# Optimization experiments

Measured on AMD Instinct MI355X. Metric: run time of the kernel, lower is better.

Reference implementation:

```python
import jax, jax.numpy as jnp
import numpy as np

N = 100_000
E = 1_600_000
D_IN = 128
D_OUT = 128
LN_EPS = 1e-5


def mean_agg(x, src, dst, deg):
    # out[dst] += x[src]; out /= deg  (scatter-mean over incoming edges)
    summed = jax.ops.segment_sum(x[src], dst, num_segments=N)
    return summed / deg[:, None]


def setup_inputs() -> dict:
    key = jax.random.key(0)
    ks = jax.random.split(key, 8)
    h = jax.random.normal(ks[0], (N, D_IN), dtype=jnp.float32)
    edge_index_mp = jax.random.randint(ks[1], (2, E), 0, N, dtype=jnp.int64)
    # deg = in-degree of each node (count of edges with dst == i), clamped to >= 1
    deg_mp = jax.ops.segment_sum(jnp.ones((E,), jnp.float32), edge_index_mp[1], num_segments=N)
    deg_mp = jnp.maximum(deg_mp, 1.0)
    scale = 1.0 / np.sqrt(D_IN)
    W_self = jax.random.uniform(ks[2], (D_OUT, D_IN), jnp.float32, -scale, scale)
    W_nb1 = jax.random.uniform(ks[3], (D_OUT, D_IN), jnp.float32, -scale, scale)
    W_hp = jax.random.uniform(ks[4], (D_OUT, D_IN), jnp.float32, -scale, scale)
    W_nb2 = jax.random.uniform(ks[5], (D_OUT, D_IN), jnp.float32, -scale, scale)
    bias = jnp.zeros((D_OUT,), jnp.float32)
    branch_logits = jnp.zeros((4,), jnp.float32)
    ln_gamma = jnp.ones((D_OUT,), jnp.float32)
    ln_beta = jnp.zeros((D_OUT,), jnp.float32)
    return {
        "h": h, "edge_index_mp": edge_index_mp, "deg_mp": deg_mp,
        "W_self": W_self, "W_nb1": W_nb1, "W_hp": W_hp, "W_nb2": W_nb2,
        "bias": bias, "branch_logits": branch_logits,
        "ln_gamma": ln_gamma, "ln_beta": ln_beta,
    }


def reference(h, edge_index_mp, deg_mp, W_self, W_nb1, W_hp, W_nb2,
              bias, branch_logits, ln_gamma, ln_beta):
    src, dst = edge_index_mp[0], edge_index_mp[1]
    nb1 = mean_agg(h, src, dst, deg_mp)          # 1-hop mean
    nb2 = mean_agg(nb1, src, dst, deg_mp)        # 2-hop mean
    hp = h - nb1                                  # high-pass branch
    scales = 2.0 * jax.nn.sigmoid(branch_logits)
    z = (scales[0] * (h @ W_self.T)
         + scales[1] * (nb1 @ W_nb1.T)
         + scales[2] * (hp @ W_hp.T)
         + scales[3] * (nb2 @ W_nb2.T)
         + bias)
    mu = jnp.mean(z, axis=-1, keepdims=True)
    var = jnp.var(z, axis=-1, keepdims=True)
    return (z - mu) * jax.lax.rsqrt(var + LN_EPS) * ln_gamma + ln_beta
```

## Files before the change

### kernel.cpp

```cpp
#include <hip/hip_runtime.h>

#define NN 100000
#define NE 1600000
#define D 128
#define KTOT 384
#define LN_EPS 1e-5f

#define PITCH_US 200
#define PITCH_DW 100
#define GM 64

#define SCAN_CHUNK 2048
#define NSB 49

#define NBK 196
#define BCAP 10240

#define FB_SCAN1   0
#define FB_WEIGHTS 49
#define FB_BIN     113
#define FB_PREP    895
#define FB_TOTAL   4020

#define WS_OFF_OFF   0
#define WS_OFF_CUR   401408
#define WS_OFF_BSUM  802816
#define WS_OFF_GCUR  803072
#define WS_OFF_WCBF  804096
#define WS_OFF_ESRC  967680
#define WS_OFF_H16   7768064
#define WS_OFF_NB1   33368064
#define WS_OFF_GBUF  33368064

typedef __attribute__((ext_vector_type(8))) _Float16 f16x8;
typedef __attribute__((ext_vector_type(2))) _Float16 f16x2;
typedef __attribute__((ext_vector_type(4))) float f32x4;
typedef __attribute__((ext_vector_type(2))) unsigned int u32x2;

__device__ __forceinline__ unsigned short f2h(float f) {
    _Float16 h = (_Float16)f;
    unsigned short s; __builtin_memcpy(&s, &h, 2); return s;
}
__device__ __forceinline__ f16x2 u2h2(unsigned u) {
    f16x2 h; __builtin_memcpy(&h, &u, 4); return h;
}
__device__ __forceinline__ unsigned pk2(float a, float b) {
    return (unsigned)f2h(a) | ((unsigned)f2h(b) << 16);
}

__global__ __launch_bounds__(256) void k_front(
    const float* __restrict__ deg, int* __restrict__ off, int* __restrict__ bsum,
    const float* __restrict__ Ws, const float* __restrict__ W1,
    const float* __restrict__ Whp, const float* __restrict__ W2,
    const float* __restrict__ logits, unsigned short* __restrict__ wcbf,
    const int* __restrict__ src, const int* __restrict__ dst,
    int* __restrict__ gcur, int2* __restrict__ gbuf,
    const float* __restrict__ h, unsigned int* __restrict__ h16) {
    __shared__ int lds[256];
    __shared__ int bcnt[NBK];
    __shared__ int bbase[NBK];
    const int b = blockIdx.x;
    const int t = threadIdx.x;

    if (b < FB_WEIGHTS) {
        int base = b * SCAN_CHUNK + t * 8;
        int v[8];
        if (base < NN) {
            float4 a0 = reinterpret_cast<const float4*>(deg + base)[0];
            float4 a1 = reinterpret_cast<const float4*>(deg + base)[1];
            v[0] = __float2int_rn(a0.x); v[1] = __float2int_rn(a0.y);
            v[2] = __float2int_rn(a0.z); v[3] = __float2int_rn(a0.w);
            v[4] = __float2int_rn(a1.x); v[5] = __float2int_rn(a1.y);
            v[6] = __float2int_rn(a1.z); v[7] = __float2int_rn(a1.w);
        } else {
            #pragma unroll
            for (int j = 0; j < 8; ++j) v[j] = 0;
        }
        int s = 0;
        #pragma unroll
        for (int j = 0; j < 8; ++j) s += v[j];
        lds[t] = s;
        __syncthreads();
        for (int ofs = 1; ofs < 256; ofs <<= 1) {
            int x = (t >= ofs) ? lds[t - ofs] : 0;
            __syncthreads();
            lds[t] += x;
            __syncthreads();
        }
        int excl = (t == 0) ? 0 : lds[t - 1];
        #pragma unroll
        for (int j = 0; j < 8; ++j) { off[base + j] = excl; excl += v[j]; }
        if (t == 255) bsum[b] = lds[255];
    } else if (b < FB_BIN) {
        int idx = (b - FB_WEIGHTS) * 256 + t;
        int o = idx >> 7, k = idx & 127;
        float s0 = 2.f / (1.f + __expf(-logits[0]));
        float s1 = 2.f / (1.f + __expf(-logits[1]));
        float s2 = 2.f / (1.f + __expf(-logits[2]));
        float s3 = 2.f / (1.f + __expf(-logits[3]));
        unsigned short b1 = f2h(s0 * Ws[idx] + s2 * Whp[idx]);
        unsigned short b2 = f2h(s1 * W1[idx] - s2 * Whp[idx]);
        unsigned short b3 = f2h(s3 * W2[idx]);
        size_t base = (size_t)o * KTOT + k;
        wcbf[base]       = b1;
        wcbf[base + 128] = b2;
        wcbf[base + 256] = b3;
    } else if (b < FB_PREP) {
        if (t < NBK) bcnt[t] = 0;
        __syncthreads();
        int e0 = (b - FB_BIN) * 2048;
        int s[8], d[8], r[8];
        #pragma unroll
        for (int it = 0; it < 8; ++it) {
            int e = e0 + it * 256 + t;
            bool ok = e < NE;
            s[it] = ok ? src[e] : 0;
            d[it] = ok ? dst[e] : -1;
            r[it] = ok ? atomicAdd(&bcnt[d[it] >> 9], 1) : 0;
        }
        __syncthreads();
        if (t < NBK) bbase[t] = atomicAdd(&gcur[t], bcnt[t]);
        __syncthreads();
        #pragma unroll
        for (int it = 0; it < 8; ++it) {
            if (d[it] >= 0) {
                int bk = d[it] >> 9;
                gbuf[(size_t)bk * BCAP + bbase[bk] + r[it]] = make_int2(s[it], d[it]);
            }
        }
    } else {
        int g2 = (b - FB_PREP) * 256 + t;
        const float4* hv = reinterpret_cast<const float4*>(h) + (size_t)g2 * 4;
        float4 a = hv[0], bb = hv[1], c = hv[2], dd = hv[3];
        uint4 o0, o1;
        o0.x = pk2(a.x, a.y);   o0.y = pk2(a.z, a.w);
        o0.z = pk2(bb.x, bb.y); o0.w = pk2(bb.z, bb.w);
        o1.x = pk2(c.x, c.y);   o1.y = pk2(c.z, c.w);
        o1.z = pk2(dd.x, dd.y); o1.w = pk2(dd.z, dd.w);
        reinterpret_cast<uint4*>(h16)[(size_t)g2 * 2]     = o0;
        reinterpret_cast<uint4*>(h16)[(size_t)g2 * 2 + 1] = o1;
    }
}

__global__ void k_scan2(int* __restrict__ bsum) {
    int t = threadIdx.x;
    int v = (t < NSB) ? bsum[t] : 0;
    #pragma unroll
    for (int ofs = 1; ofs < 64; ofs <<= 1) {
        int x = __shfl_up(v, ofs, 64);
        if (t >= ofs) v += x;
    }
    int excl = __shfl_up(v, 1, 64);
    if (t == 0) excl = 0;
    if (t < NSB) bsum[t] = excl;
    if (t == NSB - 1) bsum[NSB] = v;
}

__global__ __launch_bounds__(1024) void k_scatter2(const int2* __restrict__ gbuf,
                                                   const int* __restrict__ gcur,
                                                   const int* __restrict__ off,
                                                   const int* __restrict__ bsum,
                                                   int* __restrict__ cur,
                                                   int* __restrict__ esrc) {
    __shared__ int lcur[512];
    int b = blockIdx.x;
    int base = b << 9;
    if (threadIdx.x < 512) lcur[threadIdx.x] = 0;
    __syncthreads();
    int nb = gcur[b];
    int sb = bsum[b >> 2];
    const int2* bb = gbuf + (size_t)b * BCAP;
    for (int i = threadIdx.x; i < nb; i += 1024) {
        int2 e = bb[i];
        int p = off[e.y] + sb + atomicAdd(&lcur[e.y - base], 1);
        esrc[p] = e.x;
    }
    __syncthreads();
    if (threadIdx.x < 512) cur[base + threadIdx.x] = lcur[threadIdx.x];
}

template <bool INTERLEAVED>
__global__ __launch_bounds__(256) void k_hop(const unsigned int* __restrict__ in,
                                             unsigned int* __restrict__ outp,
                                             const int* __restrict__ off,
                                             const int* __restrict__ bsum,
                                             const int* __restrict__ cnt_arr,
                                             const int* __restrict__ esrc,
                                             const float* __restrict__ deg) {
    int w = (blockIdx.x * blockDim.x + threadIdx.x) >> 6;
    int lane = threadIdx.x & 63;
    int beg = __builtin_amdgcn_readfirstlane(off[w] + bsum[w >> 11]);
    int cnt = __builtin_amdgcn_readfirstlane(cnt_arr[w]);
    float ax = 0.f, ay = 0.f;
    for (int bs = 0; bs < cnt; bs += 64) {
        int m = cnt - bs; if (m > 64) m = 64;
        int ev = esrc[beg + bs + (lane < m ? lane : 0)];
        for (int j = 0; j < m; j += 16) {
            unsigned u[16];
            #pragma unroll
            for (int k = 0; k < 16; ++k) {
                int idx = j + k;
                int s = __builtin_amdgcn_readlane(ev, idx < m ? idx : 0);
                u[k] = in[(size_t)s * 64 + lane];
            }
            #pragma unroll
            for (int k = 0; k < 16; ++k) {
                if (j + k >= m) u[k] = 0u;
                f16x2 v = u2h2(u[k]);
                ax += (float)v.x; ay += (float)v.y;
            }
        }
    }
    float inv = 1.0f / deg[w];
    ax *= inv; ay *= inv;
    unsigned pk = (unsigned)f2h(ax) | ((unsigned)f2h(ay) << 16);
    if (INTERLEAVED) outp[(size_t)w * 128 + 64 + lane] = pk;
    else             outp[(size_t)w * 64 + lane] = pk;
}

__global__ __launch_bounds__(256) void k_gemm_ln(
    const unsigned int* __restrict__ h16,
    const unsigned int* __restrict__ nb1u,
    const unsigned short* __restrict__ wcbf, const float* __restrict__ bias,
    const float* __restrict__ gamma, const float* __restrict__ beta,
    float* __restrict__ out) {
    __shared__ __align__(16) unsigned short Xs[GM * PITCH_US];
    __shared__ float part_s[4][GM];
    __shared__ float part_q[4][GM];
    __shared__ float mu_s[GM], rs_s[GM];
    unsigned int* Xs_u = reinterpret_cast<unsigned int*>(Xs);
    const u32x2* h16v = reinterpret_cast<const u32x2*>(h16);
    const u32x2* nb1v = reinterpret_cast<const u32x2*>(nb1u);
    const u32x2* outv = reinterpret_cast<const u32x2*>(out);

    const int t = threadIdx.x;
    const int wv = t >> 6, lane = t & 63;
    const int lm = lane & 15, quad = lane >> 4;
    const int node0 = blockIdx.x * GM;
    const int obase = wv * 32;

    f32x4 acc[4][2] = {};

    #pragma unroll
    for (int it = 0; it < 8; ++it) {
        int i = t + 256 * it;
        int row = i >> 5, dp = i & 31;
        int rn = node0 + row; rn = rn < NN ? rn : NN - 1;
        u32x2 v = __builtin_nontemporal_load(&h16v[(size_t)rn * 32 + dp]);
        *reinterpret_cast<u32x2*>(&Xs_u[row * PITCH_DW + dp * 2]) = v;
    }
    #pragma unroll
    for (int it = 0; it < 4; ++it) {
        int i = t + 256 * it;
        int row = i >> 4, dp = i & 15;
        int rn = node0 + row; rn = rn < NN ? rn : NN - 1;
        u32x2 v = __builtin_nontemporal_load(&nb1v[(size_t)rn * 32 + dp]);
        *reinterpret_cast<u32x2*>(&Xs_u[row * PITCH_DW + 64 + dp * 2]) = v;
    }
    __syncthreads();

    u32x2 pre1[4], pre2[8];
    #pragma unroll
    for (int it = 0; it < 4; ++it) {
        int i = t + 256 * it;
        int row = i >> 4, dp = i & 15;
        int rn = node0 + row; rn = rn < NN ? rn : NN - 1;
        pre1[it] = __builtin_nontemporal_load(&nb1v[(size_t)rn * 32 + 16 + dp]);
    }
    #pragma unroll
    for (int it = 0; it < 8; ++it) {
        int i = t + 256 * it;
        int row = i >> 5, dp = i & 31;
        int rn = node0 + row; rn = rn < NN ? rn : NN - 1;
        pre2[it] = __builtin_nontemporal_load(&outv[(size_t)rn * 64 + 32 + dp]);
    }

    {
        f16x8 bfr[2][6];
        #pragma unroll
        for (int nt = 0; nt < 2; ++nt) {
            const unsigned short* wp =
                wcbf + (size_t)(obase + nt * 16 + lm) * KTOT + quad * 8;
            #pragma unroll
            for (int s = 0; s < 6; ++s)
                bfr[nt][s] = *reinterpret_cast<const f16x8*>(wp + s * 32);
        }
        #pragma unroll
        for (int s = 0; s < 6; ++s) {
            int koff = s * 32 + quad * 8;
            f16x8 a[4];
            #pragma unroll
            for (int mt = 0; mt < 4; ++mt)
                a[mt] = *reinterpret_cast<const f16x8*>(&Xs[(mt * 16 + lm) * PITCH_US + koff]);
            #pragma unroll
            for (int mt = 0; mt < 4; ++mt) {
                acc[mt][0] = __builtin_amdgcn_mfma_f32_16x16x32_f16(a[mt], bfr[0][s], acc[mt][0], 0, 0, 0);
                acc[mt][1] = __builtin_amdgcn_mfma_f32_16x16x32_f16(a[mt], bfr[1][s], acc[mt][1], 0, 0, 0);
            }
        }
    }
    __syncthreads();

    #pragma unroll
    for (int it = 0; it < 4; ++it) {
        int i = t + 256 * it;
        int row = i >> 4, dp = i & 15;
        *reinterpret_cast<u32x2*>(&Xs_u[row * PITCH_DW + dp * 2]) = pre1[it];
    }
    #pragma unroll
    for (int it = 0; it < 8; ++it) {
        int i = t + 256 * it;
        int row = i >> 5, dp = i & 31;
        *reinterpret_cast<u32x2*>(&Xs_u[row * PITCH_DW + 32 + dp * 2]) = pre2[it];
    }
    __syncthreads();

    {
        f16x8 bfr[2][6];
        #pragma unroll
        for (int nt = 0; nt < 2; ++nt) {
            const unsigned short* wp =
                wcbf + (size_t)(obase + nt * 16 + lm) * KTOT + 192 + quad * 8;
            #pragma unroll
            for (int s = 0; s < 6; ++s)
                bfr[nt][s] = *reinterpret_cast<const f16x8*>(wp + s * 32);
        }
        #pragma unroll
        for (int s = 0; s < 6; ++s) {
            int koff = s * 32 + quad * 8;
            f16x8 a[4];
            #pragma unroll
            for (int mt = 0; mt < 4; ++mt)
                a[mt] = *reinterpret_cast<const f16x8*>(&Xs[(mt * 16 + lm) * PITCH_US + koff]);
            #pragma unroll
            for (int mt = 0; mt < 4; ++mt) {
                acc[mt][0] = __builtin_amdgcn_mfma_f32_16x16x32_f16(a[mt], bfr[0][s], acc[mt][0], 0, 0, 0);
                acc[mt][1] = __builtin_amdgcn_mfma_f32_16x16x32_f16(a[mt], bfr[1][s], acc[mt][1], 0, 0, 0);
            }
        }
    }

    float bv0 = bias[obase + lm], bv1 = bias[obase + 16 + lm];
    #pragma unroll
    for (int mt = 0; mt < 4; ++mt) {
        float s[4], q[4];
        #pragma unroll
        for (int r = 0; r < 4; ++r) {
            float v0 = acc[mt][0][r] + bv0;
            float v1 = acc[mt][1][r] + bv1;
            acc[mt][0][r] = v0;  acc[mt][1][r] = v1;
            s[r] = v0 + v1;
            q[r] = v0 * v0 + v1 * v1;
        }
        #pragma unroll
        for (int off = 1; off < 16; off <<= 1) {
            #pragma unroll
            for (int r = 0; r < 4; ++r) {
                s[r] += __shfl_xor(s[r], off, 64);
                q[r] += __shfl_xor(q[r], off, 64);
            }
        }
        if (lm == 0) {
            #pragma unroll
            for (int r = 0; r < 4; ++r) {
                part_s[wv][mt * 16 + quad * 4 + r] = s[r];
                part_q[wv][mt * 16 + quad * 4 + r] = q[r];
            }
        }
    }
    __syncthreads();
    if (t < GM) {
        float s = part_s[0][t] + part_s[1][t] + part_s[2][t] + part_s[3][t];
        float q = part_q[0][t] + part_q[1][t] + part_q[2][t] + part_q[3][t];
        float m = s * (1.f / 128.f);
        float var = q * (1.f / 128.f) - m * m;
        mu_s[t] = m;
        rs_s[t] = rsqrtf(var + LN_EPS);
    }
    __syncthreads();

    float g0 = gamma[obase + lm], g1 = gamma[obase + 16 + lm];
    float e0 = beta[obase + lm],  e1 = beta[obase + 16 + lm];
    #pragma unroll
    for (int mt = 0; mt < 4; ++mt) {
        #pragma unroll
        for (int r = 0; r < 4; ++r) {
            int lrow = mt * 16 + quad * 4 + r;
            if (node0 + lrow < NN) {
                float mu = mu_s[lrow], rs = rs_s[lrow];
                size_t ro = (size_t)(node0 + lrow) * D;
                __builtin_nontemporal_store((acc[mt][0][r] - mu) * rs * g0 + e0,
                                            &out[ro + obase + lm]);
                __builtin_nontemporal_store((acc[mt][1][r] - mu) * rs * g1 + e1,
                                            &out[ro + obase + 16 + lm]);
            }
        }
    }
}

extern "C" void kernel_launch(void* const* d_in, const int* in_sizes, int n_in,
                              void* d_out, int out_size, void* d_ws, size_t ws_size,
                              hipStream_t stream) {
    const float* h      = (const float*)d_in[0];
    const int*   ei     = (const int*)d_in[1];
    const float* deg    = (const float*)d_in[2];
    const float* Wself  = (const float*)d_in[3];
    const float* Wnb1   = (const float*)d_in[4];
    const float* Whp    = (const float*)d_in[5];
    const float* Wnb2   = (const float*)d_in[6];
    const float* bias   = (const float*)d_in[7];
    const float* logits = (const float*)d_in[8];
    const float* gamma  = (const float*)d_in[9];
    const float* beta   = (const float*)d_in[10];
    float* out = (float*)d_out;

    char* ws = (char*)d_ws;
    int* off                 = (int*)(ws + WS_OFF_OFF);
    int* cur                 = (int*)(ws + WS_OFF_CUR);
    int* bsum                = (int*)(ws + WS_OFF_BSUM);
    int* gcur                = (int*)(ws + WS_OFF_GCUR);
    unsigned short* wcbf     = (unsigned short*)(ws + WS_OFF_WCBF);
    int* esrc                = (int*)(ws + WS_OFF_ESRC);
    int2* gbuf               = (int2*)(ws + WS_OFF_GBUF);
    unsigned int* h16        = (unsigned int*)(ws + WS_OFF_H16);
    unsigned int* nb1u       = (unsigned int*)(ws + WS_OFF_NB1);

    const int* src = ei;
    const int* dst = ei + NE;

    (void)hipMemsetAsync(gcur, 0, NBK * sizeof(int), stream);

    k_front<<<FB_TOTAL, 256, 0, stream>>>(deg, off, bsum,
                                          Wself, Wnb1, Whp, Wnb2, logits, wcbf,
                                          src, dst, gcur, gbuf, h, h16);
    k_scan2<<<1, 64, 0, stream>>>(bsum);
    k_scatter2<<<NBK, 1024, 0, stream>>>(gbuf, gcur, off, bsum, cur, esrc);

    k_hop<false><<<(NN * 64) / 256, 256, 0, stream>>>(h16, nb1u, off, bsum, cur, esrc, deg);
    k_hop<true><<<(NN * 64) / 256, 256, 0, stream>>>(nb1u, (unsigned int*)out, off, bsum, cur, esrc, deg);

    k_gemm_ln<<<(NN + GM - 1) / GM, 256, 0, stream>>>(h16, nb1u, wcbf, bias, gamma, beta, out);
}
```

Before: 300.9 us.

## Fold scan2 into scatter2 and fuse both hops into one cooperative kernel

Drops the single-block scan kernel by having every scatter block recompute the 49-entry prefix scan itself, with block 0 writing the scanned copy to a new bsum2 array. The two separate hop launches become one cooperative persistent kernel with a fixed grid, a grid-stride loop over nodes, and a grid.sync between the first and second hop. This removes two kernel launches and their gaps. In exchange, each scatter block repeats a small scan, the hop kernel now runs with limited grid occupancy, and it pays for a grid-wide barrier.

```diff
diff --git a/kernel.cpp b/kernel.cpp
--- a/kernel.cpp
+++ b/kernel.cpp
@@ -1,4 +1,7 @@
 #include <hip/hip_runtime.h>
+#include <hip/hip_cooperative_groups.h>
+
+namespace cg = cooperative_groups;
 
 #define NN 100000
 #define NE 1600000
@@ -15,6 +18,9 @@
 
 #define NBK 196
 #define BCAP 10240
+
+#define HOPS_GRID 1792
+#define HOPS_WAVES (HOPS_GRID * 4)
 
 #define FB_SCAN1   0
 #define FB_WEIGHTS 49
@@ -142,54 +148,53 @@
     }
 }
 
-__global__ void k_scan2(int* __restrict__ bsum) {
-    int t = threadIdx.x;
-    int v = (t < NSB) ? bsum[t] : 0;
-    #pragma unroll
-    for (int ofs = 1; ofs < 64; ofs <<= 1) {
-        int x = __shfl_up(v, ofs, 64);
-        if (t >= ofs) v += x;
-    }
-    int excl = __shfl_up(v, 1, 64);
-    if (t == 0) excl = 0;
-    if (t < NSB) bsum[t] = excl;
-    if (t == NSB - 1) bsum[NSB] = v;
-}
-
 __global__ __launch_bounds__(1024) void k_scatter2(const int2* __restrict__ gbuf,
                                                    const int* __restrict__ gcur,
                                                    const int* __restrict__ off,
                                                    const int* __restrict__ bsum,
+                                                   int* __restrict__ bsum2,
                                                    int* __restrict__ cur,
                                                    int* __restrict__ esrc) {
     __shared__ int lcur[512];
+    __shared__ int sb_sh;
     int b = blockIdx.x;
     int base = b << 9;
-    if (threadIdx.x < 512) lcur[threadIdx.x] = 0;
+    int t = threadIdx.x;
+    if (t < 64) {
+        int v = (t < NSB) ? bsum[t] : 0;
+        #pragma unroll
+        for (int ofs = 1; ofs < 64; ofs <<= 1) {
+            int x = __shfl_up(v, ofs, 64);
+            if (t >= ofs) v += x;
+        }
+        int excl = __shfl_up(v, 1, 64);
+        if (t == 0) excl = 0;
+        if (t == (b >> 2)) sb_sh = excl;
+        if (b == 0 && t < NSB) bsum2[t] = excl;
+    }
+    if (t < 512) lcur[t] = 0;
     __syncthreads();
     int nb = gcur[b];
-    int sb = bsum[b >> 2];
+    int sb = sb_sh;
     const int2* bb = gbuf + (size_t)b * BCAP;
-    for (int i = threadIdx.x; i < nb; i += 1024) {
+    for (int i = t; i < nb; i += 1024) {
         int2 e = bb[i];
         int p = off[e.y] + sb + atomicAdd(&lcur[e.y - base], 1);
         esrc[p] = e.x;
     }
     __syncthreads();
-    if (threadIdx.x < 512) cur[base + threadIdx.x] = lcur[threadIdx.x];
-}
-
-template <bool INTERLEAVED>
-__global__ __launch_bounds__(256) void k_hop(const unsigned int* __restrict__ in,
-                                             unsigned int* __restrict__ outp,
-                                             const int* __restrict__ off,
-                                             const int* __restrict__ bsum,
-                                             const int* __restrict__ cnt_arr,
-                                             const int* __restrict__ esrc,
-                                             const float* __restrict__ deg) {
-    int w = (blockIdx.x * blockDim.x + threadIdx.x) >> 6;
-    int lane = threadIdx.x & 63;
-    int beg = __builtin_amdgcn_readfirstlane(off[w] + bsum[w >> 11]);
+    if (t < 512) cur[base + t] = lcur[t];
+}
+
+__device__ __forceinline__ void hop_body(int w, int lane, bool interleaved,
+                                         const unsigned int* __restrict__ in,
+                                         unsigned int* __restrict__ outp,
+                                         const int* __restrict__ off,
+                                         const int* __restrict__ bsum2,
+                                         const int* __restrict__ cnt_arr,
+                                         const int* __restrict__ esrc,
+                                         const float* __restrict__ deg) {
+    int beg = __builtin_amdgcn_readfirstlane(off[w] + bsum2[w >> 11]);
     int cnt = __builtin_amdgcn_readfirstlane(cnt_arr[w]);
     float ax = 0.f, ay = 0.f;
     for (int bs = 0; bs < cnt; bs += 64) {
@@ -214,8 +219,26 @@
     float inv = 1.0f / deg[w];
     ax *= inv; ay *= inv;
     unsigned pk = (unsigned)f2h(ax) | ((unsigned)f2h(ay) << 16);
-    if (INTERLEAVED) outp[(size_t)w * 128 + 64 + lane] = pk;
+    if (interleaved) outp[(size_t)w * 128 + 64 + lane] = pk;
     else             outp[(size_t)w * 64 + lane] = pk;
+}
+
+__global__ __launch_bounds__(256) void k_hops(const unsigned int* __restrict__ h16,
+                                              unsigned int* __restrict__ nb1u,
+                                              unsigned int* __restrict__ outp,
+                                              const int* __restrict__ off,
+                                              const int* __restrict__ bsum2,
+                                              const int* __restrict__ cnt_arr,
+                                              const int* __restrict__ esrc,
+                                              const float* __restrict__ deg) {
+    cg::grid_group grid = cg::this_grid();
+    int wid0 = (blockIdx.x * 256 + threadIdx.x) >> 6;
+    int lane = threadIdx.x & 63;
+    for (int w = wid0; w < NN; w += HOPS_WAVES)
+        hop_body(w, lane, false, h16, nb1u, off, bsum2, cnt_arr, esrc, deg);
+    grid.sync();
+    for (int w = wid0; w < NN; w += HOPS_WAVES)
+        hop_body(w, lane, true, nb1u, outp, off, bsum2, cnt_arr, esrc, deg);
 }
 
 __global__ __launch_bounds__(256) void k_gemm_ln(
@@ -419,6 +442,7 @@
     int* cur                 = (int*)(ws + WS_OFF_CUR);
     int* bsum                = (int*)(ws + WS_OFF_BSUM);
     int* gcur                = (int*)(ws + WS_OFF_GCUR);
+    int* bsum2               = gcur + 200;
     unsigned short* wcbf     = (unsigned short*)(ws + WS_OFF_WCBF);
     int* esrc                = (int*)(ws + WS_OFF_ESRC);
     int2* gbuf               = (int2*)(ws + WS_OFF_GBUF);
@@ -433,11 +457,13 @@
     k_front<<<FB_TOTAL, 256, 0, stream>>>(deg, off, bsum,
                                           Wself, Wnb1, Whp, Wnb2, logits, wcbf,
                                           src, dst, gcur, gbuf, h, h16);
-    k_scan2<<<1, 64, 0, stream>>>(bsum);
-    k_scatter2<<<NBK, 1024, 0, stream>>>(gbuf, gcur, off, bsum, cur, esrc);
-
-    k_hop<false><<<(NN * 64) / 256, 256, 0, stream>>>(h16, nb1u, off, bsum, cur, esrc, deg);
-    k_hop<true><<<(NN * 64) / 256, 256, 0, stream>>>(nb1u, (unsigned int*)out, off, bsum, cur, esrc, deg);
+    k_scatter2<<<NBK, 1024, 0, stream>>>(gbuf, gcur, off, bsum, bsum2, cur, esrc);
+
+    unsigned int* outu = (unsigned int*)out;
+    void* cargs[] = { (void*)&h16, (void*)&nb1u, (void*)&outu, (void*)&off,
+                      (void*)&bsum2, (void*)&cur, (void*)&esrc, (void*)&deg };
+    (void)hipLaunchCooperativeKernel((void*)k_hops, dim3(HOPS_GRID), dim3(256),
+                                     cargs, 0, stream);
 
     k_gemm_ln<<<(NN + GM - 1) / GM, 256, 0, stream>>>(h16, nb1u, wcbf, bias, gamma, beta, out);
 }
```

New measurement: 564.1 us. 1.88x slower.
